# Kernel optimization log

Hardware: AMD Instinct MI355X
Metric: run time of the kernel (lower is better)

The kernel has to match this reference:

```python
import jax, jax.numpy as jnp
import numpy as np

EPS = 1e-5

def conv2d(x, w, b, stride, pad):
    y = jax.lax.conv_general_dilated(x, w, (stride, stride), [(pad, pad), (pad, pad)],
                                     dimension_numbers=('NCHW', 'OIHW', 'NCHW'))
    return y + b[None, :, None, None]

def _sample(xb, py, px):
    # xb: [C,H,W]; py,px: [K,Ho,Wo] fractional sample coords (zero padding outside)
    H, W = xb.shape[1], xb.shape[2]
    y0 = jnp.floor(py); x0 = jnp.floor(px)
    ay = py - y0; ax = px - x0
    y0i = y0.astype(jnp.int32); x0i = x0.astype(jnp.int32)
    out = jnp.zeros((xb.shape[0],) + py.shape, xb.dtype)
    for dy, wy in ((0, 1.0 - ay), (1, ay)):
        for dx, wx in ((0, 1.0 - ax), (1, ax)):
            yi = y0i + dy; xi = x0i + dx
            valid = (yi >= 0) & (yi < H) & (xi >= 0) & (xi < W)
            v = xb[:, jnp.clip(yi, 0, H - 1), jnp.clip(xi, 0, W - 1)]  # [C,K,Ho,Wo]
            out = out + v * (wy * wx * valid)[None]
    return out

def deform_conv2d(x, w, offset, mask, stride, pad):
    # torchvision.ops.deform_conv2d semantics (modulated, 1 offset group)
    B, C, H, W = x.shape
    Co, Ci, kh, kw = w.shape
    K = kh * kw
    Ho = (H + 2 * pad - kh) // stride + 1
    Wo = (W + 2 * pad - kw) // stride + 1
    ky, kx = jnp.meshgrid(jnp.arange(kh), jnp.arange(kw), indexing='ij')
    ky = ky.reshape(K).astype(x.dtype); kx = kx.reshape(K).astype(x.dtype)
    off = offset.reshape(B, K, 2, Ho, Wo)  # channel 2k = dy, 2k+1 = dx
    base_y = (jnp.arange(Ho) * stride - pad).astype(x.dtype)
    base_x = (jnp.arange(Wo) * stride - pad).astype(x.dtype)
    py = base_y[None, None, :, None] + ky[None, :, None, None] + off[:, :, 0]
    px = base_x[None, None, None, :] + kx[None, :, None, None] + off[:, :, 1]
    cols = jax.vmap(_sample)(x, py, px)        # [B,C,K,Ho,Wo]
    cols = cols * mask[:, None]                # modulated
    return jnp.einsum('bckhw,ock->bohw', cols, w.reshape(Co, Ci, K))

def deform_layer(x, off_w, off_b, mod_w, mod_b, w, stride, pad):
    offset = conv2d(x, off_w, off_b, stride, pad)
    mask = 2.0 * jax.nn.sigmoid(conv2d(x, mod_w, mod_b, stride, pad))
    return deform_conv2d(x, w, offset, mask, stride, pad)

def bn(x, g, b, m, v):
    return (x - m[None, :, None, None]) * (g / jnp.sqrt(v + EPS))[None, :, None, None] + b[None, :, None, None]

def prelu(x, alpha):
    return jnp.where(x > 0, x, alpha[None, :, None, None] * x)

def setup_inputs() -> dict:
    key = jax.random.key(0)
    ks = jax.random.split(key, 24)
    B, C, D, H, W, k = 4, 128, 128, 128, 128, 3
    K = k * k
    n = lambda i, shp, s: jax.random.normal(ks[i], shp, dtype=jnp.float32) * s
    inp = {
        'x': n(0, (B, C, H, W), 1.0),
        'bn1_g': 1.0 + n(1, (C,), 0.05), 'bn1_b': n(2, (C,), 0.05),
        'bn1_m': n(3, (C,), 0.1), 'bn1_v': jax.random.uniform(ks[4], (C,), jnp.float32, 0.5, 1.5),
        'off1_w': n(5, (2 * K, C, k, k), 0.01), 'off1_b': n(6, (2 * K,), 0.01),
        'mod1_w': n(7, (K, C, k, k), 0.01), 'mod1_b': n(8, (K,), 0.01),
        'w1': n(9, (D, C, k, k), 1.0 / np.sqrt(C * K)),
        'alpha': jnp.full((D,), 0.25, jnp.float32),
        'off2_w': n(10, (2 * K, D, k, k), 0.01), 'off2_b': n(11, (2 * K,), 0.01),
        'mod2_w': n(12, (K, D, k, k), 0.01), 'mod2_b': n(13, (K,), 0.01),
        'w2': n(14, (D, D, k, k), 1.0 / np.sqrt(D * K)),
        'bn2_g': 1.0 + n(15, (D,), 0.05), 'bn2_b': n(16, (D,), 0.05),
        'bn2_m': n(17, (D,), 0.1), 'bn2_v': jax.random.uniform(ks[18], (D,), jnp.float32, 0.5, 1.5),
    }
    return inp

def reference(x, bn1_g, bn1_b, bn1_m, bn1_v, off1_w, off1_b, mod1_w, mod1_b, w1, alpha,
              off2_w, off2_b, mod2_w, mod2_b, w2, bn2_g, bn2_b, bn2_m, bn2_v):
    # in_channel == depth, stride == 1 -> shortcut is MaxPool2d(1,1) == identity
    shortcut = x
    r = bn(x, bn1_g, bn1_b, bn1_m, bn1_v)
    r = deform_layer(r, off1_w, off1_b, mod1_w, mod1_b, w1, 1, 1)
    r = prelu(r, alpha)
    r = deform_layer(r, off2_w, off2_b, mod2_w, mod2_b, w2, 1, 1)
    r = bn(r, bn2_g, bn2_b, bn2_m, bn2_v)
    return r + shortcut
```

## Files before the change

### kernel.cpp

```cpp
#include <hip/hip_runtime.h>
#include <hip/hip_bf16.h>
#include <hip/hip_fp16.h>
#include <math.h>

#define DEV_INLINE __device__ __forceinline__

typedef __attribute__((ext_vector_type(8))) short short8;
typedef __attribute__((ext_vector_type(8))) unsigned short ushort8v;
typedef __attribute__((ext_vector_type(4))) float f32x4;

constexpr int H = 128, W = 128, C = 128, B = 4;
constexpr int KK = 9;
constexpr int KT2 = 1184;

DEV_INLINE unsigned short f2bf(float f) {
  union { float f; unsigned u; } v; v.f = f;
  unsigned r = v.u + 0x7FFFu + ((v.u >> 16) & 1u);
  return (unsigned short)(r >> 16);
}
DEV_INLINE float ubits(unsigned u) {
  union { unsigned u; float f; } v; v.u = u; return v.f;
}
DEV_INLINE unsigned pack2bf(float a, float b) {
  float2 t; t.x = a; t.y = b;
  __hip_bfloat162 h = __float22bfloat162_rn(t);
  union { __hip_bfloat162 h; unsigned u; } c; c.h = h;
  return c.u;
}
DEV_INLINE unsigned f2h2(float a, float b) {
  __half2 h = __floats2half2_rn(a, b);
  union { __half2 h; unsigned u; } c; c.h = h;
  return c.u;
}
DEV_INLINE float2 h2f2(unsigned u) {
  union { unsigned u; __half2 h; } c; c.u = u;
  return __half22float2(c.h);
}
DEV_INLINE unsigned xblend(unsigned L, unsigned R, float wA, float wB) {
  const float l0 = ubits(L << 16), l1 = ubits(L & 0xFFFF0000u);
  const float r0 = ubits(R << 16), r1 = ubits(R & 0xFFFF0000u);
  return f2h2(wA * l0 + wB * r0, wA * l1 + wB * r1);
}
DEV_INLINE void gload_lds16(const unsigned short* g, unsigned short* l) {
  __builtin_amdgcn_global_load_lds(
      (const __attribute__((address_space(1))) unsigned*)g,
      (__attribute__((address_space(3))) unsigned*)l, 16, 0, 0);
}

template<int LAYER>
__global__ __launch_bounds__(256, 4)
void fusedL(const unsigned short* __restrict__ src,
            const unsigned short* __restrict__ wOM,
            const unsigned short* __restrict__ wS,
            const float* __restrict__ bias,
            const float* __restrict__ pA, const float* __restrict__ pB,
            const float* __restrict__ pM, const float* __restrict__ pV,
            const float* __restrict__ resid,
            unsigned short* __restrict__ outh,
            float* __restrict__ outf)
{
  constexpr bool BN   = (LAYER == 1);
  constexpr int  NCH3 = BN ? 37 : 36;
  __shared__ __attribute__((aligned(16))) char smem[39680];
  float* sOff = (float*)smem;
  unsigned short* aBuf0 = (unsigned short*)smem;
  unsigned short* aBuf1 = (unsigned short*)(smem + 8192);
  char* gBase = smem + 16384;
  unsigned* sTabU = (unsigned*)(smem + 32768);

  const int tid  = threadIdx.x;
  const int lane = tid & 63;
  const int m16  = lane & 15;
  const int q    = lane >> 4;
  const int wv   = tid >> 6;

  const int raw  = blockIdx.x;
  const int xcd  = raw & 7;
  const int slot = raw >> 3;
  const int b    = xcd >> 1;
  const int hy   = ((xcd & 1) << 6) | (slot >> 1);
  const int hx0  = (slot & 1) << 6;
  const unsigned short* __restrict__ srcB = src + ((size_t)b << 14) * C;

  const int pos = (wv << 4) + m16;
  const int hx  = hx0 + pos;
  const int cbq = q << 3;
  const int ppos = tid >> 2;
  const int ps   = tid & 3;

  f32x4 acc2[2];
  acc2[0] = (f32x4){0.f, 0.f, 0.f, 0.f};
  acc2[1] = (f32x4){0.f, 0.f, 0.f, 0.f};

  ushort8v pv;
  bool pvok;
  {
    const int iy = hy - 1, ix = hx - 1;
    pvok = ((unsigned)iy < (unsigned)H) && ((unsigned)ix < (unsigned)W);
    const int rb = pvok ? (iy * W + ix) : 0;
    pv = *(const ushort8v*)(srcB + ((size_t)rb * C + cbq));
  }
  short8 pa0 = *(const short8*)(wOM + (size_t)lane * 8);
  short8 pa1 = *(const short8*)(wOM + (size_t)lane * 8 + 512);

  #pragma unroll 1
  for (int ch = 0; ch < 36; ++ch) {
    const short8 a0 = pa0, a1 = pa1;
    if (ch + 1 < 36) {
      const unsigned short* ap = wOM + ((size_t)((ch + 1) * 128 + lane)) * 8;
      pa0 = *(const short8*)(ap);
      pa1 = *(const short8*)(ap + 512);
    }
    ushort8v nv = pv;
    bool nok = false;
    if (ch + 1 < 36) {
      const int tapn = (ch + 1) >> 2, cgn = (ch + 1) & 3;
      const int ky = tapn / 3, kx = tapn - 3 * (tapn / 3);
      const int iy = hy + ky - 1;
      const int ix = hx + kx - 1;
      nok = ((unsigned)iy < (unsigned)H) && ((unsigned)ix < (unsigned)W);
      const int rb = nok ? (iy * W + ix) : 0;
      nv = *(const ushort8v*)(srcB + ((size_t)rb * C + (cgn << 5) + cbq));
    }
    union { ushort8v v; unsigned u[4]; short8 s; } bfr;
    bfr.v = pv;
    if (!pvok) { bfr.u[0] = 0; bfr.u[1] = 0; bfr.u[2] = 0; bfr.u[3] = 0; }
    acc2[0] = __builtin_amdgcn_mfma_f32_16x16x32_bf16(a0, bfr.s, acc2[0], 0, 0, 0);
    acc2[1] = __builtin_amdgcn_mfma_f32_16x16x32_bf16(a1, bfr.s, acc2[1], 0, 0, 0);
    pv = nv; pvok = nok;
  }
  if constexpr (BN) {
    union { unsigned u[4]; short8 s; } bfr;
    float sv[8];
    #pragma unroll
    for (int j = 0; j < 8; ++j) {
      const int kj = cbq + j;
      float s = 0.f;
      if (kj < KK) {
        const int ky = kj / 3, kx = kj - 3 * (kj / 3);
        const int iy = hy + ky - 1, ix = hx + kx - 1;
        s = (((unsigned)iy < (unsigned)H) && ((unsigned)ix < (unsigned)W)) ? 1.f : 0.f;
      }
      sv[j] = s;
    }
    #pragma unroll
    for (int t = 0; t < 4; ++t) bfr.u[t] = pack2bf(sv[2 * t], sv[2 * t + 1]);
    const unsigned short* ap = wOM + ((size_t)36 * 128 + lane) * 8;
    acc2[0] = __builtin_amdgcn_mfma_f32_16x16x32_bf16(*(const short8*)(ap), bfr.s, acc2[0], 0, 0, 0);
    acc2[1] = __builtin_amdgcn_mfma_f32_16x16x32_bf16(*(const short8*)(ap + 512), bfr.s, acc2[1], 0, 0, 0);
  }
  #pragma unroll
  for (int ot = 0; ot < 2; ++ot) {
    #pragma unroll
    for (int rg = 0; rg < 4; ++rg) {
      const int o = ot * 16 + (q << 2) + rg;
      if (o < 27) {
        float v = acc2[ot][rg] + bias[o];
        if (o >= 18) v = 2.f / (1.f + expf(-v));
        sOff[pos * 29 + o] = v;
      }
    }
  }
  __syncthreads();

  unsigned bnB0 = 0, bnB1 = 0, bnB2 = 0, bnB3 = 0;
  {
    float tSum[9];
    const float* myOff = sOff + pos * 29;
    #pragma unroll
    for (int tap = 0; tap < 9; ++tap) {
      const int ky = tap / 3, kx = tap - 3 * (tap / 3);
      const float oy = myOff[2 * tap];
      const float ox = myOff[2 * tap + 1];
      const float mv = myOff[18 + tap];
      const float py = (float)(hy - 1 + ky) + oy;
      const float px = (float)(hx - 1 + kx) + ox;
      const float fy = floorf(py), fx = floorf(px);
      const float ay = py - fy, ax = px - fx;
      const int y0 = (int)fy, x0 = (int)fx;
      const int y1 = y0 + 1, x1 = x0 + 1;
      const float wyt = (1.f - ay) * (((unsigned)y0 < (unsigned)H) ? 1.f : 0.f);
      const float wyb = ay * (((unsigned)y1 < (unsigned)H) ? 1.f : 0.f);
      const int y0c = min(max(y0, 0), H - 1), y1c = min(max(y1, 0), H - 1);
      const int bx  = min(max(x0, 0), W - 2);
      float wA = 0.f, wB = 0.f;
      if (x0 == bx)          { wA = 1.f - ax; wB = ax; }
      else if (x1 == bx)     { wA = ax; }
      else if (x0 == bx + 1) { wB = 1.f - ax; }
      if (q == 0) {
        const int tb = (tap * 64 + pos) * 3;
        sTabU[tb + 0] = (unsigned)(y0c * W + bx) | ((unsigned)(y1c * W + bx) << 16);
        sTabU[tb + 1] = f2h2(wA, wB);
        sTabU[tb + 2] = f2h2(mv * wyt, mv * wyb);
      }
      tSum[tap] = mv * (wyt + wyb) * (wA + wB);
    }
    if constexpr (BN) {
      float sv[8];
      #pragma unroll
      for (int j = 0; j < 8; ++j) {
        float s = 0.f;
        if (q == 0) s = tSum[j];
        else if (q == 1 && j == 0) s = tSum[8];
        sv[j] = s;
      }
      bnB0 = pack2bf(sv[0], sv[1]); bnB1 = pack2bf(sv[2], sv[3]);
      bnB2 = pack2bf(sv[4], sv[5]); bnB3 = pack2bf(sv[6], sv[7]);
    }
  }
  __syncthreads();

  f32x4 acc[8];
  #pragma unroll
  for (int i = 0; i < 8; ++i) acc[i] = (f32x4){0.f, 0.f, 0.f, 0.f};

  {
    unsigned short* dst0 = aBuf0 + (wv << 9);
    gload_lds16(wS + (size_t)tid * 8, dst0);
    gload_lds16(wS + (size_t)(256 + tid) * 8, dst0 + 2048);
  }
  unsigned idP  = sTabU[ppos * 3 + 0];
  unsigned wabP = sTabU[ppos * 3 + 1];
  {
    const unsigned short* aT = srcB + (size_t)(idP & 0xFFFFu) * C + ps * 8;
    const unsigned short* aB = srcB + (size_t)(idP >> 16) * C + ps * 8;
    union { uint4 v; unsigned u[4]; } LT, RT, LB, RB, oT, oB;
    LT.v = *(const uint4*)(aT); RT.v = *(const uint4*)(aT + C);
    LB.v = *(const uint4*)(aB); RB.v = *(const uint4*)(aB + C);
    const float2 wab = h2f2(wabP);
    #pragma unroll
    for (int d = 0; d < 4; ++d) {
      oT.u[d] = xblend(LT.u[d], RT.u[d], wab.x, wab.y);
      oB.u[d] = xblend(LB.u[d], RB.u[d], wab.x, wab.y);
    }
    char* gd = gBase + ppos * 64 + (ps << 4);
    *(uint4*)gd = oT.v;
    *(uint4*)(gd + 4096) = oB.v;
  }
  __syncthreads();

  unsigned wYc = sTabU[pos * 3 + 2];
  #pragma unroll 1
  for (int tap = 0; tap < 9; ++tap) {
    const float2 wY = h2f2(wYc);
    #pragma unroll
    for (int cg = 0; cg < 4; ++cg) {
      const int ch = (tap << 2) + cg;
      const int p  = ch & 1;
      const bool morew = (ch + 1 < NCH3);
      const bool morep = (ch + 1 < 36);
      if (morew) {
        unsigned short* wd = ((cg + 1) & 1) ? aBuf1 : aBuf0;
        unsigned short* dst = wd + (wv << 9);
        const size_t gb = (size_t)(ch + 1) * 4096;
        gload_lds16(wS + gb + (size_t)tid * 8, dst);
        gload_lds16(wS + gb + (size_t)(256 + tid) * 8, dst + 2048);
      }
      if (cg == 3 && tap < 8) {
        idP  = sTabU[((tap + 1) * 64 + ppos) * 3 + 0];
        wabP = sTabU[((tap + 1) * 64 + ppos) * 3 + 1];
      }
      union { uint4 v; unsigned u[4]; } LT, RT, LB, RB;
      if (morep) {
        const int cbn = ((cg + 1) & 3) << 5;
        const unsigned short* aT = srcB + (size_t)(idP & 0xFFFFu) * C + cbn + ps * 8;
        const unsigned short* aB = srcB + (size_t)(idP >> 16) * C + cbn + ps * 8;
        LT.v = *(const uint4*)(aT); RT.v = *(const uint4*)(aT + C);
        LB.v = *(const uint4*)(aB); RB.v = *(const uint4*)(aB + C);
      }
      union { uint4 v; unsigned u[4]; } Tb, Bb;
      Tb.v = *(const uint4*)(gBase + p * 8192 +        pos * 64 + (q << 4));
      Bb.v = *(const uint4*)(gBase + p * 8192 + 4096 + pos * 64 + (q << 4));
      union { unsigned u[4]; short8 s; } bfr;
      #pragma unroll
      for (int d = 0; d < 4; ++d) {
        const float2 tf = h2f2(Tb.u[d]);
        const float2 bf = h2f2(Bb.u[d]);
        bfr.u[d] = pack2bf(wY.x * tf.x + wY.y * bf.x,
                           wY.x * tf.y + wY.y * bf.y);
      }
      const unsigned short* rbuf = p ? aBuf1 : aBuf0;
      #pragma unroll
      for (int ot = 0; ot < 8; ++ot) {
        const short8 afr = *(const short8*)(rbuf + ((size_t)(ot * 64 + lane)) * 8);
        acc[ot] = __builtin_amdgcn_mfma_f32_16x16x32_bf16(afr, bfr.s, acc[ot], 0, 0, 0);
      }
      if (morep) {
        const float2 wab = h2f2(wabP);
        union { uint4 v; unsigned u[4]; } oT, oB;
        #pragma unroll
        for (int d = 0; d < 4; ++d) {
          oT.u[d] = xblend(LT.u[d], RT.u[d], wab.x, wab.y);
          oB.u[d] = xblend(LB.u[d], RB.u[d], wab.x, wab.y);
        }
        char* gd = gBase + (p ^ 1) * 8192 + ppos * 64 + (ps << 4);
        *(uint4*)gd = oT.v;
        *(uint4*)(gd + 4096) = oB.v;
      }
      __syncthreads();
    }
    if (tap < 8) wYc = sTabU[((tap + 1) * 64 + pos) * 3 + 2];
  }

  if constexpr (BN) {
    union { unsigned u[4]; short8 s; } bfr;
    bfr.u[0] = bnB0; bfr.u[1] = bnB1; bfr.u[2] = bnB2; bfr.u[3] = bnB3;
    #pragma unroll
    for (int ot = 0; ot < 8; ++ot) {
      const short8 afr = *(const short8*)(aBuf0 + ((size_t)(ot * 64 + lane)) * 8);
      acc[ot] = __builtin_amdgcn_mfma_f32_16x16x32_bf16(afr, bfr.s, acc[ot], 0, 0, 0);
    }
  }

  #pragma unroll
  for (int ot = 0; ot < 8; ++ot) {
    if constexpr (LAYER == 1) {
      const float a0 = pA[ot * 16 + (q << 2) + 0];
      const float a1 = pA[ot * 16 + (q << 2) + 1];
      const float a2 = pA[ot * 16 + (q << 2) + 2];
      const float a3 = pA[ot * 16 + (q << 2) + 3];
      const float v0 = acc[ot][0], v1 = acc[ot][1];
      const float v2 = acc[ot][2], v3 = acc[ot][3];
      uint2 st;
      st.x = pack2bf(v0 > 0.f ? v0 : a0 * v0, v1 > 0.f ? v1 : a1 * v1);
      st.y = pack2bf(v2 > 0.f ? v2 : a2 * v2, v3 > 0.f ? v3 : a3 * v3);
      const int n = (b << 14) + hy * W + hx;
      *(uint2*)(outh + (size_t)n * C + ot * 16 + (q << 2)) = st;
    } else {
      #pragma unroll
      for (int rg = 0; rg < 4; ++rg) {
        const int o = ot * 16 + (q << 2) + rg;
        const float vv = acc[ot][rg];
        const size_t oi = (((size_t)(b * C + o)) << 14) + hy * W + hx;
        const float s  = pA[o] * rsqrtf(pV[o] + 1e-5f);
        const float sh = pB[o] - pM[o] * s;
        outf[oi] = vv * s + sh + resid[oi];
      }
    }
  }
}

__global__ __launch_bounds__(256, 4)
void xcvt3(const float* __restrict__ x, unsigned short* __restrict__ xb)
{
  __shared__ unsigned tile[64 * 69];
  const int b   = blockIdx.y;
  const int p0  = blockIdx.x * 64;
  const int tid = threadIdx.x;
  const int pl  = tid & 63;
  const int cg  = tid >> 6;
  const float* __restrict__ xp = x + (((size_t)(b * C) + cg * 32) << 14) + p0 + pl;
  #pragma unroll
  for (int j = 0; j < 16; ++j) {
    const float a = xp[(size_t)(2 * j) << 14];
    const float c = xp[(size_t)(2 * j + 1) << 14];
    tile[pl * 69 + cg * 16 + j] = pack2bf(a, c);
  }
  __syncthreads();
  const int pl2 = tid >> 2;
  const int cq  = tid & 3;
  unsigned* dst = (unsigned*)(xb + (((size_t)(b << 14)) + p0 + pl2) * C + cq * 32);
  #pragma unroll
  for (int k = 0; k < 16; k += 4) {
    uint4 v;
    v.x = tile[pl2 * 69 + cq * 16 + k];
    v.y = tile[pl2 * 69 + cq * 16 + k + 1];
    v.z = tile[pl2 * 69 + cq * 16 + k + 2];
    v.w = tile[pl2 * 69 + cq * 16 + k + 3];
    *(uint4*)(dst + k) = v;
  }
}

__global__ void prep5(const float* __restrict__ w1, const float* __restrict__ w2,
                      const float* __restrict__ ow1, const float* __restrict__ mw1,
                      const float* __restrict__ ob1, const float* __restrict__ mb1,
                      const float* __restrict__ ow2, const float* __restrict__ mw2,
                      const float* __restrict__ ob2, const float* __restrict__ mb2,
                      const float* __restrict__ g, const float* __restrict__ bb,
                      const float* __restrict__ m, const float* __restrict__ v,
                      unsigned short* __restrict__ wb1, unsigned short* __restrict__ wb2,
                      unsigned short* __restrict__ wom1, unsigned short* __restrict__ wom2,
                      float* __restrict__ bias1, float* __restrict__ bias2)
{
  const int i = blockIdx.x * 256 + threadIdx.x;
  if (i < 128 * KT2) {
    const int j = i & 7, lane = (i >> 3) & 63, ot = (i >> 9) & 7, ch = i >> 12;
    const int o = ot * 16 + (lane & 15);
    const int qj = ((lane >> 4) << 3) + j;
    unsigned short v1 = 0, v2 = 0;
    if (ch < 36) {
      const int tap = ch >> 2;
      const int c   = ((ch & 3) << 5) + qj;
      const float s = g[c] * rsqrtf(v[c] + 1e-5f);
      v1 = f2bf(w1[(size_t)(o * 128 + c) * 9 + tap] * s);
      v2 = f2bf(w2[(size_t)(o * 128 + c) * 9 + tap]);
    } else if (qj < KK) {
      float acc = 0.f;
      for (int c = 0; c < 128; ++c) {
        const float s  = g[c] * rsqrtf(v[c] + 1e-5f);
        const float sh = bb[c] - m[c] * s;
        acc += w1[(size_t)(o * 128 + c) * 9 + qj] * sh;
      }
      v1 = f2bf(acc);
    }
    wb1[i] = v1; wb2[i] = v2;
  }
  if (i < 32 * KT2) {
    const int j = i & 7, lane = (i >> 3) & 63, ot = (i >> 9) & 1, ch = i >> 10;
    const int o = ot * 16 + (lane & 15);
    const int qj = ((lane >> 4) << 3) + j;
    unsigned short v1 = 0, v2 = 0;
    if (ch < 36) {
      const int tap = ch >> 2;
      const int c   = ((ch & 3) << 5) + qj;
      const float s = g[c] * rsqrtf(v[c] + 1e-5f);
      if (o < 18) {
        v1 = f2bf(ow1[(size_t)(o * 128 + c) * 9 + tap] * s);
        v2 = f2bf(ow2[(size_t)(o * 128 + c) * 9 + tap]);
      } else if (o < 27) {
        v1 = f2bf(mw1[(size_t)((o - 18) * 128 + c) * 9 + tap] * s);
        v2 = f2bf(mw2[(size_t)((o - 18) * 128 + c) * 9 + tap]);
      }
    } else if (qj < KK && o < 27) {
      const float* wsrc = (o < 18) ? ow1 + (size_t)o * 1152
                                   : mw1 + (size_t)(o - 18) * 1152;
      float acc = 0.f;
      for (int c = 0; c < 128; ++c) {
        const float s  = g[c] * rsqrtf(v[c] + 1e-5f);
        const float sh = bb[c] - m[c] * s;
        acc += wsrc[(size_t)c * 9 + qj] * sh;
      }
      v1 = f2bf(acc);
    }
    wom1[i] = v1; wom2[i] = v2;
  }
  if (i < 32) {
    float b1 = 0.f, b2 = 0.f;
    if (i < 18)      { b1 = ob1[i];      b2 = ob2[i]; }
    else if (i < 27) { b1 = mb1[i - 18]; b2 = mb2[i - 18]; }
    bias1[i] = b1; bias2[i] = b2;
  }
}

extern "C" void kernel_launch(void* const* d_in, const int* in_sizes, int n_in,
                              void* d_out, int out_size, void* d_ws, size_t ws_size,
                              hipStream_t stream)
{
  const float* x     = (const float*)d_in[0];
  const float* bn1g  = (const float*)d_in[1];
  const float* bn1b  = (const float*)d_in[2];
  const float* bn1m  = (const float*)d_in[3];
  const float* bn1v  = (const float*)d_in[4];
  const float* ow1   = (const float*)d_in[5];
  const float* ob1   = (const float*)d_in[6];
  const float* mw1   = (const float*)d_in[7];
  const float* mb1   = (const float*)d_in[8];
  const float* w1    = (const float*)d_in[9];
  const float* alpha = (const float*)d_in[10];
  const float* ow2   = (const float*)d_in[11];
  const float* ob2   = (const float*)d_in[12];
  const float* mw2   = (const float*)d_in[13];
  const float* mb2   = (const float*)d_in[14];
  const float* w2    = (const float*)d_in[15];
  const float* bn2g  = (const float*)d_in[16];
  const float* bn2b  = (const float*)d_in[17];
  const float* bn2m  = (const float*)d_in[18];
  const float* bn2v  = (const float*)d_in[19];
  float* out = (float*)d_out;

  char* wsp = (char*)d_ws;
  unsigned short* xbf  = (unsigned short*)(wsp);
  unsigned short* r2bf = (unsigned short*)(wsp + 16777216);
  unsigned short* wb1  = (unsigned short*)(wsp + 40632320);
  unsigned short* wb2  = (unsigned short*)(wsp + 40935424);
  unsigned short* wom1 = (unsigned short*)(wsp + 41238528);
  unsigned short* wom2 = (unsigned short*)(wsp + 41314304);
  float* bias1 = (float*)(wsp + 41390080);
  float* bias2 = (float*)(wsp + 41390208);

  xcvt3<<<dim3(256, 4), 256, 0, stream>>>(x, xbf);
  prep5<<<(128 * KT2 + 255) / 256, 256, 0, stream>>>(
      w1, w2, ow1, mw1, ob1, mb1, ow2, mw2, ob2, mb2,
      bn1g, bn1b, bn1m, bn1v, wb1, wb2, wom1, wom2, bias1, bias2);

  fusedL<1><<<1024, 256, 0, stream>>>(xbf, wom1, wb1, bias1, alpha,
      nullptr, nullptr, nullptr, nullptr, r2bf, nullptr);
  fusedL<2><<<1024, 256, 0, stream>>>(r2bf, wom2, wb2, bias2, bn2g,
      bn2b, bn2m, bn2v, x, nullptr, out);
}
```

Baseline: 304.3 us.

## Restage deformable-conv gather as full bilinear blend with per-wave output-channel tiling

```diff
diff --git a/kernel.cpp b/kernel.cpp
--- a/kernel.cpp
+++ b/kernel.cpp
@@ -12,6 +12,8 @@
 constexpr int H = 128, W = 128, C = 128, B = 4;
 constexpr int KK = 9;
 constexpr int KT2 = 1184;
+constexpr int GP = 80;
+constexpr int GHALF = 64 * GP;
 
 DEV_INLINE unsigned short f2bf(float f) {
   union { float f; unsigned u; } v; v.f = f;
@@ -36,10 +38,13 @@
   union { unsigned u; __half2 h; } c; c.u = u;
   return __half22float2(c.h);
 }
-DEV_INLINE unsigned xblend(unsigned L, unsigned R, float wA, float wB) {
-  const float l0 = ubits(L << 16), l1 = ubits(L & 0xFFFF0000u);
-  const float r0 = ubits(R << 16), r1 = ubits(R & 0xFFFF0000u);
-  return f2h2(wA * l0 + wB * r0, wA * l1 + wB * r1);
+DEV_INLINE unsigned blend4(unsigned TL, unsigned TR, unsigned BL, unsigned BR,
+                           float w00, float w01, float w10, float w11) {
+  const float lo = w00 * ubits(TL << 16) + w01 * ubits(TR << 16)
+                 + w10 * ubits(BL << 16) + w11 * ubits(BR << 16);
+  const float hi = w00 * ubits(TL & 0xFFFF0000u) + w01 * ubits(TR & 0xFFFF0000u)
+                 + w10 * ubits(BL & 0xFFFF0000u) + w11 * ubits(BR & 0xFFFF0000u);
+  return pack2bf(lo, hi);
 }
 DEV_INLINE void gload_lds16(const unsigned short* g, unsigned short* l) {
   __builtin_amdgcn_global_load_lds(
@@ -61,12 +66,12 @@
 {
   constexpr bool BN   = (LAYER == 1);
   constexpr int  NCH3 = BN ? 37 : 36;
-  __shared__ __attribute__((aligned(16))) char smem[39680];
+  __shared__ __attribute__((aligned(16))) char smem[33536];
   float* sOff = (float*)smem;
   unsigned short* aBuf0 = (unsigned short*)smem;
   unsigned short* aBuf1 = (unsigned short*)(smem + 8192);
-  char* gBase = smem + 16384;
-  unsigned* sTabU = (unsigned*)(smem + 32768);
+  char* gBuf = smem + 16384;
+  unsigned* sTabU = (unsigned*)(smem + 26624);
 
   const int tid  = threadIdx.x;
   const int lane = tid & 63;
@@ -82,9 +87,7 @@
   const int hx0  = (slot & 1) << 6;
   const unsigned short* __restrict__ srcB = src + ((size_t)b << 14) * C;
 
-  const int pos = (wv << 4) + m16;
-  const int hx  = hx0 + pos;
-  const int cbq = q << 3;
+  const int pos  = (wv << 4) + m16;
   const int ppos = tid >> 2;
   const int ps   = tid & 3;
 
@@ -92,16 +95,16 @@
   acc2[0] = (f32x4){0.f, 0.f, 0.f, 0.f};
   acc2[1] = (f32x4){0.f, 0.f, 0.f, 0.f};
 
-  ushort8v pv;
-  bool pvok;
   {
-    const int iy = hy - 1, ix = hx - 1;
-    pvok = ((unsigned)iy < (unsigned)H) && ((unsigned)ix < (unsigned)W);
-    const int rb = pvok ? (iy * W + ix) : 0;
-    pv = *(const ushort8v*)(srcB + ((size_t)rb * C + cbq));
+    const int iy = hy - 1, ix = hx0 + ppos - 1;
+    uint4 v; v.x = 0; v.y = 0; v.z = 0; v.w = 0;
+    if (((unsigned)iy < (unsigned)H) && ((unsigned)ix < (unsigned)W))
+      v = *(const uint4*)(srcB + (size_t)(iy * W + ix) * C + (ps << 3));
+    *(uint4*)(gBuf + ppos * GP + (ps << 4)) = v;
   }
   short8 pa0 = *(const short8*)(wOM + (size_t)lane * 8);
   short8 pa1 = *(const short8*)(wOM + (size_t)lane * 8 + 512);
+  __syncthreads();
 
   #pragma unroll 1
   for (int ch = 0; ch < 36; ++ch) {
@@ -111,34 +114,33 @@
       pa0 = *(const short8*)(ap);
       pa1 = *(const short8*)(ap + 512);
     }
-    ushort8v nv = pv;
-    bool nok = false;
+    uint4 nv; nv.x = 0; nv.y = 0; nv.z = 0; nv.w = 0;
     if (ch + 1 < 36) {
       const int tapn = (ch + 1) >> 2, cgn = (ch + 1) & 3;
       const int ky = tapn / 3, kx = tapn - 3 * (tapn / 3);
       const int iy = hy + ky - 1;
-      const int ix = hx + kx - 1;
-      nok = ((unsigned)iy < (unsigned)H) && ((unsigned)ix < (unsigned)W);
-      const int rb = nok ? (iy * W + ix) : 0;
-      nv = *(const ushort8v*)(srcB + ((size_t)rb * C + (cgn << 5) + cbq));
-    }
-    union { ushort8v v; unsigned u[4]; short8 s; } bfr;
-    bfr.v = pv;
-    if (!pvok) { bfr.u[0] = 0; bfr.u[1] = 0; bfr.u[2] = 0; bfr.u[3] = 0; }
-    acc2[0] = __builtin_amdgcn_mfma_f32_16x16x32_bf16(a0, bfr.s, acc2[0], 0, 0, 0);
-    acc2[1] = __builtin_amdgcn_mfma_f32_16x16x32_bf16(a1, bfr.s, acc2[1], 0, 0, 0);
-    pv = nv; pvok = nok;
+      const int ix = hx0 + ppos + kx - 1;
+      if (((unsigned)iy < (unsigned)H) && ((unsigned)ix < (unsigned)W))
+        nv = *(const uint4*)(srcB + (size_t)(iy * W + ix) * C + (cgn << 5) + (ps << 3));
+    }
+    const short8 bfrg = *(const short8*)(gBuf + (ch & 1) * GHALF + pos * GP + (q << 4));
+    acc2[0] = __builtin_amdgcn_mfma_f32_16x16x32_bf16(a0, bfrg, acc2[0], 0, 0, 0);
+    acc2[1] = __builtin_amdgcn_mfma_f32_16x16x32_bf16(a1, bfrg, acc2[1], 0, 0, 0);
+    if (ch + 1 < 36) {
+      *(uint4*)(gBuf + ((ch + 1) & 1) * GHALF + ppos * GP + (ps << 4)) = nv;
+      __syncthreads();
+    }
   }
   if constexpr (BN) {
     union { unsigned u[4]; short8 s; } bfr;
     float sv[8];
     #pragma unroll
     for (int j = 0; j < 8; ++j) {
-      const int kj = cbq + j;
+      const int kj = (q << 3) + j;
       float s = 0.f;
       if (kj < KK) {
         const int ky = kj / 3, kx = kj - 3 * (kj / 3);
-        const int iy = hy + ky - 1, ix = hx + kx - 1;
+        const int iy = hy + ky - 1, ix = hx0 + pos + kx - 1;
         s = (((unsigned)iy < (unsigned)H) && ((unsigned)ix < (unsigned)W)) ? 1.f : 0.f;
       }
       sv[j] = s;
@@ -149,6 +151,7 @@
     acc2[0] = __builtin_amdgcn_mfma_f32_16x16x32_bf16(*(const short8*)(ap), bfr.s, acc2[0], 0, 0, 0);
     acc2[1] = __builtin_amdgcn_mfma_f32_16x16x32_bf16(*(const short8*)(ap + 512), bfr.s, acc2[1], 0, 0, 0);
   }
+  __syncthreads();
   #pragma unroll
   for (int ot = 0; ot < 2; ++ot) {
     #pragma unroll
@@ -163,9 +166,7 @@
   }
   __syncthreads();
 
-  unsigned bnB0 = 0, bnB1 = 0, bnB2 = 0, bnB3 = 0;
   {
-    float tSum[9];
     const float* myOff = sOff + pos * 29;
     #pragma unroll
     for (int tap = 0; tap < 9; ++tap) {
@@ -174,7 +175,7 @@
       const float ox = myOff[2 * tap + 1];
       const float mv = myOff[18 + tap];
       const float py = (float)(hy - 1 + ky) + oy;
-      const float px = (float)(hx - 1 + kx) + ox;
+      const float px = (float)(hx0 + pos - 1 + kx) + ox;
       const float fy = floorf(py), fx = floorf(px);
       const float ay = py - fy, ax = px - fx;
       const int y0 = (int)fy, x0 = (int)fx;
@@ -190,151 +191,146 @@
       if (q == 0) {
         const int tb = (tap * 64 + pos) * 3;
         sTabU[tb + 0] = (unsigned)(y0c * W + bx) | ((unsigned)(y1c * W + bx) << 16);
-        sTabU[tb + 1] = f2h2(wA, wB);
-        sTabU[tb + 2] = f2h2(mv * wyt, mv * wyb);
-      }
-      tSum[tap] = mv * (wyt + wyb) * (wA + wB);
-    }
-    if constexpr (BN) {
-      float sv[8];
-      #pragma unroll
-      for (int j = 0; j < 8; ++j) {
-        float s = 0.f;
-        if (q == 0) s = tSum[j];
-        else if (q == 1 && j == 0) s = tSum[8];
-        sv[j] = s;
-      }
-      bnB0 = pack2bf(sv[0], sv[1]); bnB1 = pack2bf(sv[2], sv[3]);
-      bnB2 = pack2bf(sv[4], sv[5]); bnB3 = pack2bf(sv[6], sv[7]);
-    }
-  }
-  __syncthreads();
-
-  f32x4 acc[8];
+        sTabU[tb + 1] = f2h2(mv * wyt * wA, mv * wyt * wB);
+        sTabU[tb + 2] = f2h2(mv * wyb * wA, mv * wyb * wB);
+      }
+    }
+  }
+  __syncthreads();
+
+  f32x4 acc[2][4];
   #pragma unroll
-  for (int i = 0; i < 8; ++i) acc[i] = (f32x4){0.f, 0.f, 0.f, 0.f};
+  for (int i = 0; i < 2; ++i)
+    #pragma unroll
+    for (int j = 0; j < 4; ++j) acc[i][j] = (f32x4){0.f, 0.f, 0.f, 0.f};
 
   {
     unsigned short* dst0 = aBuf0 + (wv << 9);
     gload_lds16(wS + (size_t)tid * 8, dst0);
     gload_lds16(wS + (size_t)(256 + tid) * 8, dst0 + 2048);
   }
-  unsigned idP  = sTabU[ppos * 3 + 0];
-  unsigned wabP = sTabU[ppos * 3 + 1];
+  unsigned pid, pw0, pw1;
   {
-    const unsigned short* aT = srcB + (size_t)(idP & 0xFFFFu) * C + ps * 8;
-    const unsigned short* aB = srcB + (size_t)(idP >> 16) * C + ps * 8;
-    union { uint4 v; unsigned u[4]; } LT, RT, LB, RB, oT, oB;
-    LT.v = *(const uint4*)(aT); RT.v = *(const uint4*)(aT + C);
-    LB.v = *(const uint4*)(aB); RB.v = *(const uint4*)(aB + C);
-    const float2 wab = h2f2(wabP);
-    #pragma unroll
-    for (int d = 0; d < 4; ++d) {
-      oT.u[d] = xblend(LT.u[d], RT.u[d], wab.x, wab.y);
-      oB.u[d] = xblend(LB.u[d], RB.u[d], wab.x, wab.y);
-    }
-    char* gd = gBase + ppos * 64 + (ps << 4);
-    *(uint4*)gd = oT.v;
-    *(uint4*)(gd + 4096) = oB.v;
-  }
-  __syncthreads();
-
-  unsigned wYc = sTabU[pos * 3 + 2];
+    const int tb = ppos * 3;
+    pid = sTabU[tb]; pw0 = sTabU[tb + 1]; pw1 = sTabU[tb + 2];
+    const unsigned short* pT  = srcB + (size_t)(pid & 0xFFFFu) * C + (ps << 3);
+    const unsigned short* pBm = srcB + (size_t)(pid >> 16) * C + (ps << 3);
+    const uint4 TL = *(const uint4*)(pT),  TR = *(const uint4*)(pT + C);
+    const uint4 BL = *(const uint4*)(pBm), BR = *(const uint4*)(pBm + C);
+    const float2 wa = h2f2(pw0), wb = h2f2(pw1);
+    uint4 o;
+    o.x = blend4(TL.x, TR.x, BL.x, BR.x, wa.x, wa.y, wb.x, wb.y);
+    o.y = blend4(TL.y, TR.y, BL.y, BR.y, wa.x, wa.y, wb.x, wb.y);
+    o.z = blend4(TL.z, TR.z, BL.z, BR.z, wa.x, wa.y, wb.x, wb.y);
+    o.w = blend4(TL.w, TR.w, BL.w, BR.w, wa.x, wa.y, wb.x, wb.y);
+    *(uint4*)(gBuf + ppos * GP + (ps << 4)) = o;
+  }
+  __syncthreads();
+
   #pragma unroll 1
-  for (int tap = 0; tap < 9; ++tap) {
-    const float2 wY = h2f2(wYc);
-    #pragma unroll
-    for (int cg = 0; cg < 4; ++cg) {
-      const int ch = (tap << 2) + cg;
-      const int p  = ch & 1;
-      const bool morew = (ch + 1 < NCH3);
-      const bool morep = (ch + 1 < 36);
-      if (morew) {
-        unsigned short* wd = ((cg + 1) & 1) ? aBuf1 : aBuf0;
-        unsigned short* dst = wd + (wv << 9);
-        const size_t gb = (size_t)(ch + 1) * 4096;
-        gload_lds16(wS + gb + (size_t)tid * 8, dst);
-        gload_lds16(wS + gb + (size_t)(256 + tid) * 8, dst + 2048);
-      }
-      if (cg == 3 && tap < 8) {
-        idP  = sTabU[((tap + 1) * 64 + ppos) * 3 + 0];
-        wabP = sTabU[((tap + 1) * 64 + ppos) * 3 + 1];
-      }
-      union { uint4 v; unsigned u[4]; } LT, RT, LB, RB;
-      if (morep) {
-        const int cbn = ((cg + 1) & 3) << 5;
-        const unsigned short* aT = srcB + (size_t)(idP & 0xFFFFu) * C + cbn + ps * 8;
-        const unsigned short* aB = srcB + (size_t)(idP >> 16) * C + cbn + ps * 8;
-        LT.v = *(const uint4*)(aT); RT.v = *(const uint4*)(aT + C);
-        LB.v = *(const uint4*)(aB); RB.v = *(const uint4*)(aB + C);
-      }
-      union { uint4 v; unsigned u[4]; } Tb, Bb;
-      Tb.v = *(const uint4*)(gBase + p * 8192 +        pos * 64 + (q << 4));
-      Bb.v = *(const uint4*)(gBase + p * 8192 + 4096 + pos * 64 + (q << 4));
+  for (int ch = 0; ch < 36; ++ch) {
+    const int p = ch & 1;
+    const bool morew = (ch + 1 < NCH3);
+    const bool morep = (ch + 1 < 36);
+    if (morew) {
+      unsigned short* wd = ((ch + 1) & 1) ? aBuf1 : aBuf0;
+      unsigned short* dst = wd + (wv << 9);
+      const size_t gb = (size_t)(ch + 1) * 4096;
+      gload_lds16(wS + gb + (size_t)tid * 8, dst);
+      gload_lds16(wS + gb + (size_t)(256 + tid) * 8, dst + 2048);
+    }
+    if (morep && (((ch + 1) & 3) == 0)) {
+      const int tb = (((ch + 1) >> 2) * 64 + ppos) * 3;
+      pid = sTabU[tb]; pw0 = sTabU[tb + 1]; pw1 = sTabU[tb + 2];
+    }
+    uint4 TL, TR, BL, BR;
+    if (morep) {
+      const int cbn = (((ch + 1) & 3) << 5) + (ps << 3);
+      const unsigned short* pT  = srcB + (size_t)(pid & 0xFFFFu) * C + cbn;
+      const unsigned short* pBm = srcB + (size_t)(pid >> 16) * C + cbn;
+      TL = *(const uint4*)(pT);  TR = *(const uint4*)(pT + C);
+      BL = *(const uint4*)(pBm); BR = *(const uint4*)(pBm + C);
+    }
+    const unsigned short* rbuf = p ? aBuf1 : aBuf0;
+    const short8 af0 = *(const short8*)(rbuf + ((size_t)((2 * wv) * 64 + lane)) * 8);
+    const short8 af1 = *(const short8*)(rbuf + ((size_t)((2 * wv + 1) * 64 + lane)) * 8);
+    const char* gb = gBuf + p * GHALF;
+    short8 bf[4];
+    #pragma unroll
+    for (int pg = 0; pg < 4; ++pg)
+      bf[pg] = *(const short8*)(gb + (pg * 16 + m16) * GP + (q << 4));
+    #pragma unroll
+    for (int pg = 0; pg < 4; ++pg) {
+      acc[0][pg] = __builtin_amdgcn_mfma_f32_16x16x32_bf16(af0, bf[pg], acc[0][pg], 0, 0, 0);
+      acc[1][pg] = __builtin_amdgcn_mfma_f32_16x16x32_bf16(af1, bf[pg], acc[1][pg], 0, 0, 0);
+    }
+    if (morep) {
+      const float2 wa = h2f2(pw0), wb = h2f2(pw1);
+      uint4 o;
+      o.x = blend4(TL.x, TR.x, BL.x, BR.x, wa.x, wa.y, wb.x, wb.y);
+      o.y = blend4(TL.y, TR.y, BL.y, BR.y, wa.x, wa.y, wb.x, wb.y);
+      o.z = blend4(TL.z, TR.z, BL.z, BR.z, wa.x, wa.y, wb.x, wb.y);
+      o.w = blend4(TL.w, TR.w, BL.w, BR.w, wa.x, wa.y, wb.x, wb.y);
+      *(uint4*)(gBuf + (p ^ 1) * GHALF + ppos * GP + (ps << 4)) = o;
+    }
+    if (morew) __syncthreads();
+  }
+
+  if constexpr (BN) {
+    const short8 af0 = *(const short8*)(aBuf0 + ((size_t)((2 * wv) * 64 + lane)) * 8);
+    const short8 af1 = *(const short8*)(aBuf0 + ((size_t)((2 * wv + 1) * 64 + lane)) * 8);
+    #pragma unroll
+    for (int pg = 0; pg < 4; ++pg) {
+      float sv[8];
+      #pragma unroll
+      for (int j = 0; j < 8; ++j) {
+        const int k = (q << 3) + j;
+        float s = 0.f;
+        if (k < KK) {
+          const int tb = (k * 64 + pg * 16 + m16) * 3;
+          const float2 a = h2f2(sTabU[tb + 1]);
+          const float2 c = h2f2(sTabU[tb + 2]);
+          s = a.x + a.y + c.x + c.y;
+        }
+        sv[j] = s;
+      }
       union { unsigned u[4]; short8 s; } bfr;
       #pragma unroll
-      for (int d = 0; d < 4; ++d) {
-        const float2 tf = h2f2(Tb.u[d]);
-        const float2 bf = h2f2(Bb.u[d]);
-        bfr.u[d] = pack2bf(wY.x * tf.x + wY.y * bf.x,
-                           wY.x * tf.y + wY.y * bf.y);
-      }
-      const unsigned short* rbuf = p ? aBuf1 : aBuf0;
-      #pragma unroll
-      for (int ot = 0; ot < 8; ++ot) {
-        const short8 afr = *(const short8*)(rbuf + ((size_t)(ot * 64 + lane)) * 8);
-        acc[ot] = __builtin_amdgcn_mfma_f32_16x16x32_bf16(afr, bfr.s, acc[ot], 0, 0, 0);
-      }
-      if (morep) {
-        const float2 wab = h2f2(wabP);
-        union { uint4 v; unsigned u[4]; } oT, oB;
-        #pragma unroll
-        for (int d = 0; d < 4; ++d) {
-          oT.u[d] = xblend(LT.u[d], RT.u[d], wab.x, wab.y);
-          oB.u[d] = xblend(LB.u[d], RB.u[d], wab.x, wab.y);
-        }
-        char* gd = gBase + (p ^ 1) * 8192 + ppos * 64 + (ps << 4);
-        *(uint4*)gd = oT.v;
-        *(uint4*)(gd + 4096) = oB.v;
-      }
-      __syncthreads();
-    }
-    if (tap < 8) wYc = sTabU[((tap + 1) * 64 + pos) * 3 + 2];
-  }
-
-  if constexpr (BN) {
-    union { unsigned u[4]; short8 s; } bfr;
-    bfr.u[0] = bnB0; bfr.u[1] = bnB1; bfr.u[2] = bnB2; bfr.u[3] = bnB3;
-    #pragma unroll
-    for (int ot = 0; ot < 8; ++ot) {
-      const short8 afr = *(const short8*)(aBuf0 + ((size_t)(ot * 64 + lane)) * 8);
-      acc[ot] = __builtin_amdgcn_mfma_f32_16x16x32_bf16(afr, bfr.s, acc[ot], 0, 0, 0);
+      for (int t = 0; t < 4; ++t) bfr.u[t] = pack2bf(sv[2 * t], sv[2 * t + 1]);
+      acc[0][pg] = __builtin_amdgcn_mfma_f32_16x16x32_bf16(af0, bfr.s, acc[0][pg], 0, 0, 0);
+      acc[1][pg] = __builtin_amdgcn_mfma_f32_16x16x32_bf16(af1, bfr.s, acc[1][pg], 0, 0, 0);
     }
   }
 
   #pragma unroll
-  for (int ot = 0; ot < 8; ++ot) {
+  for (int oi = 0; oi < 2; ++oi) {
+    const int ot = wv * 2 + oi;
     if constexpr (LAYER == 1) {
       const float a0 = pA[ot * 16 + (q << 2) + 0];
       const float a1 = pA[ot * 16 + (q << 2) + 1];
       const float a2 = pA[ot * 16 + (q << 2) + 2];
       const float a3 = pA[ot * 16 + (q << 2) + 3];
-      const float v0 = acc[ot][0], v1 = acc[ot][1];
-      const float v2 = acc[ot][2], v3 = acc[ot][3];
-      uint2 st;
-      st.x = pack2bf(v0 > 0.f ? v0 : a0 * v0, v1 > 0.f ? v1 : a1 * v1);
-      st.y = pack2bf(v2 > 0.f ? v2 : a2 * v2, v3 > 0.f ? v3 : a3 * v3);
-      const int n = (b << 14) + hy * W + hx;
-      *(uint2*)(outh + (size_t)n * C + ot * 16 + (q << 2)) = st;
+      #pragma unroll
+      for (int pg = 0; pg < 4; ++pg) {
+        const float v0 = acc[oi][pg][0], v1 = acc[oi][pg][1];
+        const float v2 = acc[oi][pg][2], v3 = acc[oi][pg][3];
+        uint2 st;
+        st.x = pack2bf(v0 > 0.f ? v0 : a0 * v0, v1 > 0.f ? v1 : a1 * v1);
+        st.y = pack2bf(v2 > 0.f ? v2 : a2 * v2, v3 > 0.f ? v3 : a3 * v3);
+        const int n = (b << 14) + hy * W + hx0 + pg * 16 + m16;
+        *(uint2*)(outh + (size_t)n * C + ot * 16 + (q << 2)) = st;
+      }
     } else {
       #pragma unroll
       for (int rg = 0; rg < 4; ++rg) {
         const int o = ot * 16 + (q << 2) + rg;
-        const float vv = acc[ot][rg];
-        const size_t oi = (((size_t)(b * C + o)) << 14) + hy * W + hx;
         const float s  = pA[o] * rsqrtf(pV[o] + 1e-5f);
         const float sh = pB[o] - pM[o] * s;
-        outf[oi] = vv * s + sh + resid[oi];
+        #pragma unroll
+        for (int pg = 0; pg < 4; ++pg) {
+          const size_t oi2 = (((size_t)(b * C + o)) << 14) + hy * W + hx0 + pg * 16 + m16;
+          outf[oi2] = acc[oi][pg][rg] * s + sh + resid[oi2];
+        }
       }
     }
   }
```

Result: faster. 274.1 us (-9.9%).
